# Kernel optimization log

Hardware: AMD Instinct MI355X
Metric: run time of the kernel (lower is better)

The kernel has to match this reference:

```python
import jax, jax.numpy as jnp
import numpy as np
import math

L, B, E, H = 1024, 16, 512, 8
NUM_REL = 2 * L - 1  # 2047


def setup_inputs() -> dict:
    key = jax.random.key(0)
    ks = jax.random.split(key, 9)
    s = 0.02
    query = jax.random.normal(ks[0], (L, B, E), dtype=jnp.float32)
    return {
        "query": query,
        "key": jax.random.normal(ks[1], (L, B, E), dtype=jnp.float32),
        "value": jax.random.normal(ks[2], (L, B, E), dtype=jnp.float32),
        "in_proj_weight": jax.random.normal(ks[3], (3 * E, E), dtype=jnp.float32) * s,
        "in_proj_bias": jax.random.normal(ks[4], (3 * E,), dtype=jnp.float32) * s,
        "out_proj_weight": jax.random.normal(ks[5], (E, E), dtype=jnp.float32) * s,
        "out_proj_bias": jax.random.normal(ks[6], (E,), dtype=jnp.float32) * s,
        "rpe_weight_table": jax.random.normal(ks[7], (H, NUM_REL), dtype=jnp.float32) * s,
        "rpe_indices": jax.random.randint(ks[8], (L, L), 0, NUM_REL, dtype=jnp.int32),
    }


def _heads(x, w, b):
    # x: (N, Bn, E), w: (E, E), b: (E,) -> (Bn, H, N, d)
    n, bn, e = x.shape
    d = e // H
    y = jnp.einsum('nbe,fe->nbf', x, w) + b
    return y.reshape(n, bn, H, d).transpose(1, 2, 0, 3)


def reference(query, key, value, in_proj_weight, in_proj_bias, out_proj_weight,
              out_proj_bias, rpe_weight_table, rpe_indices):
    l, bn, e = query.shape
    d = e // H
    wq, wk, wv = jnp.split(in_proj_weight, 3, axis=0)
    bq, bk, bv = jnp.split(in_proj_bias, 3, axis=0)
    q = _heads(query, wq, bq)   # (B, H, L, d)
    k = _heads(key, wk, bk)     # (B, H, S, d)
    v = _heads(value, wv, bv)   # (B, H, S, d)
    q = q / math.sqrt(d)
    # rel-pos bias: gather table -> (H, L, S), broadcast over batch
    bias = rpe_weight_table[:, rpe_indices]
    attn = jnp.einsum('bhld,bhsd->bhls', q, k) + bias[None]
    attn = jax.nn.softmax(attn, axis=-1)
    out = jnp.einsum('bhls,bhsd->bhld', attn, v)   # (B, H, L, d)
    out = out.transpose(2, 0, 1, 3).reshape(l, bn, e)  # (L, B, E)
    out = jnp.einsum('lbe,fe->lbf', out, out_proj_weight) + out_proj_bias
    return out
```

## Files before the change

### kernel.cpp

```cpp
#include <hip/hip_runtime.h>
#include <hip/hip_bf16.h>


#define L_SEQ 1024
#define B_N   16
#define E_DIM 512
#define H_N   8
#define NREL  2047

typedef _Float16 f16;
using half4   = __attribute__((ext_vector_type(4))) _Float16;
using half8   = __attribute__((ext_vector_type(8))) _Float16;
using floatx4 = __attribute__((ext_vector_type(4))) float;

#define LGKM_BARRIER() do {                                   \
    asm volatile("s_waitcnt lgkmcnt(0)" ::: "memory");        \
    __builtin_amdgcn_sched_barrier(0);                        \
    __builtin_amdgcn_s_barrier();                             \
    __builtin_amdgcn_sched_barrier(0);                        \
} while (0)

__device__ __forceinline__ half4 cvt4(const float4 a) {
    half4 h;
    h[0] = (f16)a.x; h[1] = (f16)a.y; h[2] = (f16)a.z; h[3] = (f16)a.w;
    return h;
}

__global__ __launch_bounds__(256) void qkv_kernel(
    const float* __restrict__ Xq, const float* __restrict__ Xk, const float* __restrict__ Xv,
    const float* __restrict__ W, const float* __restrict__ Bias,
    f16* __restrict__ Qo, f16* __restrict__ Ko, f16* __restrict__ Vo)
{
    const int flat = blockIdx.x;
    const int xcd  = flat & 7;
    const int slot = flat >> 3;
    const int g    = xcd * 48 + (slot >> 2);
    const int f0   = (slot & 3) << 7;
    const int proj = g >> 7;
    const int n0   = (g & 127) << 7;

    const float* X  = (proj == 0) ? Xq : (proj == 1) ? Xk : Xv;
    const float* Wp = W + (size_t)(proj << 9) * E_DIM;

    __shared__ __align__(16) f16 As[2][128][40];
    __shared__ __align__(16) f16 Bs[2][128][40];

    const int tid  = threadIdx.x;
    const int w    = tid >> 6;
    const int lane = tid & 63;
    const int quad = lane >> 4, c = lane & 15;
    const int wm = (w >> 1) << 6, wn = (w & 1) << 6;

    const int srow = (w << 5) + (lane >> 3);
    const int scol = (lane & 7) << 2;
    const float* Xg = X  + (size_t)(n0 + srow) * E_DIM + scol;
    const float* Wg = Wp + (size_t)(f0 + srow) * E_DIM + scol;

    float4 lx[4], lw[4];
    auto load_tile = [&](int kk) {
#pragma unroll
        for (int i = 0; i < 4; ++i)
            lx[i] = *reinterpret_cast<const float4*>(Xg + (size_t)(i * 8) * E_DIM + kk);
#pragma unroll
        for (int i = 0; i < 4; ++i)
            lw[i] = *reinterpret_cast<const float4*>(Wg + (size_t)(i * 8) * E_DIM + kk);
    };
    auto write_tile = [&](int buf) {
#pragma unroll
        for (int i = 0; i < 4; ++i)
            *reinterpret_cast<half4*>(&As[buf][srow + i * 8][scol]) = cvt4(lx[i]);
#pragma unroll
        for (int i = 0; i < 4; ++i)
            *reinterpret_cast<half4*>(&Bs[buf][srow + i * 8][scol]) = cvt4(lw[i]);
    };

    floatx4 acc[4][4] = {};

    load_tile(0);
    write_tile(0);
    load_tile(32);
    LGKM_BARRIER();

    for (int t = 0; t < 16; ++t) {
        const int cur = t & 1;

        half8 a[4], bfr[4];
#pragma unroll
        for (int mt = 0; mt < 4; ++mt)
            a[mt] = *reinterpret_cast<const half8*>(&As[cur][wm + mt * 16 + c][quad * 8]);
#pragma unroll
        for (int nt = 0; nt < 4; ++nt)
            bfr[nt] = *reinterpret_cast<const half8*>(&Bs[cur][wn + nt * 16 + c][quad * 8]);
#pragma unroll
        for (int mt = 0; mt < 4; ++mt)
#pragma unroll
            for (int nt = 0; nt < 4; ++nt)
                acc[mt][nt] = __builtin_amdgcn_mfma_f32_16x16x32_f16(a[mt], bfr[nt], acc[mt][nt], 0, 0, 0);

        if (t < 15) {
            write_tile(cur ^ 1);
            if (t < 14) load_tile((t + 2) * 32);
        }
        LGKM_BARRIER();
    }

    f16* Dst = (proj == 0) ? Qo : (proj == 1) ? Ko : Vo;
    const float scale = (proj == 0) ? 0.125f : 1.0f;

#pragma unroll
    for (int nt = 0; nt < 4; ++nt) {
        const int fl = f0 + wn + nt * 16 + c;
        const float bj = Bias[(proj << 9) + fl];
        const int h = fl >> 6, d = fl & 63;
#pragma unroll
        for (int mt = 0; mt < 4; ++mt) {
#pragma unroll
            for (int r = 0; r < 4; ++r) {
                const int n = n0 + wm + mt * 16 + quad * 4 + r;
                const int l = n >> 4, b = n & 15;
                Dst[((((size_t)b * H_N + h) * L_SEQ + l) << 6) + d] =
                    (f16)((acc[mt][nt][r] + bj) * scale);
            }
        }
    }
}

__global__ __launch_bounds__(256) void transpose_v(
    const f16* __restrict__ V, f16* __restrict__ Vt)
{
    const int l0 = blockIdx.x << 6;
    const size_t base = (size_t)blockIdx.y << 16;
    __shared__ __align__(16) f16 T[64][72];
    const int tid = threadIdx.x;
    const int r = tid >> 2, co = (tid & 3) << 4;

    const uint4 a0 = *reinterpret_cast<const uint4*>(V + base + (size_t)(l0 + r) * 64 + co);
    const uint4 a1 = *reinterpret_cast<const uint4*>(V + base + (size_t)(l0 + r) * 64 + co + 8);
    *reinterpret_cast<uint4*>(&T[r][co])     = a0;
    *reinterpret_cast<uint4*>(&T[r][co + 8]) = a1;
    __syncthreads();

    union { f16 h[16]; uint4 u[2]; } pk;
#pragma unroll
    for (int j = 0; j < 16; ++j) pk.h[j] = T[co + j][r];
    *reinterpret_cast<uint4*>(Vt + base + (size_t)r * 1024 + l0 + co)     = pk.u[0];
    *reinterpret_cast<uint4*>(Vt + base + (size_t)r * 1024 + l0 + co + 8) = pk.u[1];
}

__global__ __launch_bounds__(256, 3) void attn_kernel(
    const f16* __restrict__ Q, const f16* __restrict__ K, const f16* __restrict__ Vt,
    const int* __restrict__ RPE, const float* __restrict__ Tab, f16* __restrict__ CTX)
{
    const int flat = blockIdx.x;
    const int xcd  = flat & 7;
    const int slot = flat >> 3;
    const int q0   = (slot & 7) << 7;
    const int bh   = ((slot >> 3) << 3) + xcd;
    const int b = bh >> 3, h = bh & 7;

    const int tid  = threadIdx.x;
    const int w    = tid >> 6;
    const int lane = tid & 63;
    const int quad = lane >> 4, c = lane & 15;

    __shared__ __align__(16) f16 Ks[64][72];
    __shared__ __align__(16) f16 Vts[64][72];
    __shared__ __align__(16) f16 Pw[4][32][72];
    __shared__ float tab[NREL];

    const size_t base = (size_t)bh << 16;

    for (int i = tid; i < NREL; i += 256) tab[i] = Tab[h * NREL + i];

    const int qg0 = q0 + (w << 5);
    half8 Aq[2][2];
#pragma unroll
    for (int s = 0; s < 2; ++s) {
        const f16* qp = Q + base + (size_t)(qg0 + s * 16 + c) * 64 + quad * 8;
        Aq[s][0] = *reinterpret_cast<const half8*>(qp);
        Aq[s][1] = *reinterpret_cast<const half8*>(qp + 32);
    }

    floatx4 o[2][4] = {};
    float l_part[2][4] = {};

    const int* rp = RPE + (size_t)(qg0 + (quad << 2)) * 1024 + c;

    const int sr = tid >> 2, so = (tid & 3) << 4;
    const f16* kbase = K  + base + (size_t)sr * 64 + so;
    const f16* vbase = Vt + base + (size_t)sr * 1024 + so;

    uint4 pk0 = *reinterpret_cast<const uint4*>(kbase);
    uint4 pk1 = *reinterpret_cast<const uint4*>(kbase + 8);
    uint4 pv0 = *reinterpret_cast<const uint4*>(vbase);
    uint4 pv1 = *reinterpret_cast<const uint4*>(vbase + 8);

    for (int j0 = 0; j0 < L_SEQ; j0 += 64) {
        __syncthreads();
        *reinterpret_cast<uint4*>(&Ks[sr][so])      = pk0;
        *reinterpret_cast<uint4*>(&Ks[sr][so + 8])  = pk1;
        *reinterpret_cast<uint4*>(&Vts[sr][so])     = pv0;
        *reinterpret_cast<uint4*>(&Vts[sr][so + 8]) = pv1;
        __syncthreads();

        if (j0 + 64 < L_SEQ) {
            const f16* kn = kbase + (size_t)(j0 + 64) * 64;
            const f16* vn = vbase + (j0 + 64);
            pk0 = *reinterpret_cast<const uint4*>(kn);
            pk1 = *reinterpret_cast<const uint4*>(kn + 8);
            pv0 = *reinterpret_cast<const uint4*>(vn);
            pv1 = *reinterpret_cast<const uint4*>(vn + 8);
        }

        int idx[2][4][4];
#pragma unroll
        for (int s = 0; s < 2; ++s)
#pragma unroll
            for (int r = 0; r < 4; ++r)
#pragma unroll
                for (int nt = 0; nt < 4; ++nt)
                    idx[s][r][nt] = rp[(size_t)(s * 16 + r) * 1024 + j0 + nt * 16];

        floatx4 sc[2][4];
#pragma unroll
        for (int nt = 0; nt < 4; ++nt) {
            const half8 b0 = *reinterpret_cast<const half8*>(&Ks[nt * 16 + c][quad * 8]);
            const half8 b1 = *reinterpret_cast<const half8*>(&Ks[nt * 16 + c][32 + quad * 8]);
            floatx4 t0 = {}, t1 = {};
            t0 = __builtin_amdgcn_mfma_f32_16x16x32_f16(Aq[0][0], b0, t0, 0, 0, 0);
            t0 = __builtin_amdgcn_mfma_f32_16x16x32_f16(Aq[0][1], b1, t0, 0, 0, 0);
            t1 = __builtin_amdgcn_mfma_f32_16x16x32_f16(Aq[1][0], b0, t1, 0, 0, 0);
            t1 = __builtin_amdgcn_mfma_f32_16x16x32_f16(Aq[1][1], b1, t1, 0, 0, 0);
            sc[0][nt] = t0; sc[1][nt] = t1;
        }

#pragma unroll
        for (int s = 0; s < 2; ++s)
#pragma unroll
            for (int r = 0; r < 4; ++r) {
                float rs = 0.0f;
#pragma unroll
                for (int nt = 0; nt < 4; ++nt) {
                    const float p = __expf(sc[s][nt][r] + tab[idx[s][r][nt]]);
                    rs += p;
                    Pw[w][s * 16 + quad * 4 + r][nt * 16 + c] = (f16)p;
                }
                l_part[s][r] += rs;
            }

        half8 vb[4][2];
#pragma unroll
        for (int nt = 0; nt < 4; ++nt) {
            vb[nt][0] = *reinterpret_cast<const half8*>(&Vts[nt * 16 + c][quad * 8]);
            vb[nt][1] = *reinterpret_cast<const half8*>(&Vts[nt * 16 + c][32 + quad * 8]);
        }
#pragma unroll
        for (int s = 0; s < 2; ++s) {
            const half8 Ap0 = *reinterpret_cast<const half8*>(&Pw[w][s * 16 + c][quad * 8]);
            const half8 Ap1 = *reinterpret_cast<const half8*>(&Pw[w][s * 16 + c][32 + quad * 8]);
#pragma unroll
            for (int nt = 0; nt < 4; ++nt) {
                o[s][nt] = __builtin_amdgcn_mfma_f32_16x16x32_f16(Ap0, vb[nt][0], o[s][nt], 0, 0, 0);
                o[s][nt] = __builtin_amdgcn_mfma_f32_16x16x32_f16(Ap1, vb[nt][1], o[s][nt], 0, 0, 0);
            }
        }
    }

#pragma unroll
    for (int s = 0; s < 2; ++s)
#pragma unroll
        for (int r = 0; r < 4; ++r) {
            float l = l_part[s][r];
            l += __shfl_xor(l, 1); l += __shfl_xor(l, 2);
            l += __shfl_xor(l, 4); l += __shfl_xor(l, 8);
            const float inv = 1.0f / l;
            const int lrow = qg0 + s * 16 + quad * 4 + r;
            f16* dp = CTX + ((size_t)(lrow * 16 + b)) * 512 + h * 64;
#pragma unroll
            for (int nt = 0; nt < 4; ++nt)
                dp[nt * 16 + c] = (f16)(o[s][nt][r] * inv);
        }
}

__global__ __launch_bounds__(256) void out_kernel(
    const f16* __restrict__ X, const float* __restrict__ W, const float* __restrict__ Bias,
    float* __restrict__ Out)
{
    const int flat = blockIdx.x;
    const int xcd  = flat & 7;
    const int slot = flat >> 3;
    const int m    = xcd * 16 + (slot >> 2);
    const int f0   = (slot & 3) << 7;
    const int n0   = m << 7;

    __shared__ __align__(16) f16 As[2][128][40];
    __shared__ __align__(16) f16 Bs[2][128][40];

    const int tid  = threadIdx.x;
    const int w    = tid >> 6;
    const int lane = tid & 63;
    const int quad = lane >> 4, c = lane & 15;
    const int wm = (w >> 1) << 6, wn = (w & 1) << 6;

    const int arow = (w << 5) + (lane >> 2);
    const int acol = (lane & 3) << 3;
    const f16* Xg = X + (size_t)(n0 + arow) * E_DIM + acol;

    const int srow = (w << 5) + (lane >> 3);
    const int scol = (lane & 7) << 2;
    const float* Wg = W + (size_t)(f0 + srow) * E_DIM + scol;

    uint4  la[2];
    float4 lw[4];
    auto load_tile = [&](int kk) {
#pragma unroll
        for (int i = 0; i < 2; ++i)
            la[i] = *reinterpret_cast<const uint4*>(Xg + (size_t)(i * 16) * E_DIM + kk);
#pragma unroll
        for (int i = 0; i < 4; ++i)
            lw[i] = *reinterpret_cast<const float4*>(Wg + (size_t)(i * 8) * E_DIM + kk);
    };
    auto write_tile = [&](int buf) {
#pragma unroll
        for (int i = 0; i < 2; ++i)
            *reinterpret_cast<uint4*>(&As[buf][arow + i * 16][acol]) = la[i];
#pragma unroll
        for (int i = 0; i < 4; ++i)
            *reinterpret_cast<half4*>(&Bs[buf][srow + i * 8][scol]) = cvt4(lw[i]);
    };

    floatx4 acc[4][4] = {};

    load_tile(0);
    write_tile(0);
    load_tile(32);
    LGKM_BARRIER();

    for (int t = 0; t < 16; ++t) {
        const int cur = t & 1;

        half8 a[4], bfr[4];
#pragma unroll
        for (int mt = 0; mt < 4; ++mt)
            a[mt] = *reinterpret_cast<const half8*>(&As[cur][wm + mt * 16 + c][quad * 8]);
#pragma unroll
        for (int nt = 0; nt < 4; ++nt)
            bfr[nt] = *reinterpret_cast<const half8*>(&Bs[cur][wn + nt * 16 + c][quad * 8]);
#pragma unroll
        for (int mt = 0; mt < 4; ++mt)
#pragma unroll
            for (int nt = 0; nt < 4; ++nt)
                acc[mt][nt] = __builtin_amdgcn_mfma_f32_16x16x32_f16(a[mt], bfr[nt], acc[mt][nt], 0, 0, 0);

        if (t < 15) {
            write_tile(cur ^ 1);
            if (t < 14) load_tile((t + 2) * 32);
        }
        LGKM_BARRIER();
    }

#pragma unroll
    for (int nt = 0; nt < 4; ++nt) {
        const int f = f0 + wn + nt * 16 + c;
        const float bj = Bias[f];
#pragma unroll
        for (int mt = 0; mt < 4; ++mt) {
#pragma unroll
            for (int r = 0; r < 4; ++r) {
                const int n = n0 + wm + mt * 16 + quad * 4 + r;
                Out[(size_t)n * E_DIM + f] = acc[mt][nt][r] + bj;
            }
        }
    }
}

extern "C" void kernel_launch(void* const* d_in, const int* in_sizes, int n_in,
                              void* d_out, int out_size, void* d_ws, size_t ws_size,
                              hipStream_t stream) {
    const float* q_in = (const float*)d_in[0];
    const float* k_in = (const float*)d_in[1];
    const float* v_in = (const float*)d_in[2];
    const float* ipw  = (const float*)d_in[3];
    const float* ipb  = (const float*)d_in[4];
    const float* opw  = (const float*)d_in[5];
    const float* opb  = (const float*)d_in[6];
    const float* tab  = (const float*)d_in[7];
    const int*   rpe  = (const int*)d_in[8];
    float* out = (float*)d_out;

    f16* ws   = (f16*)d_ws;
    f16* Q    = ws;
    f16* K    = ws + 8388608;
    f16* Vt   = ws + 16777216;
    f16* Vtmp = ws + 25165824;
    f16* CTX  = ws + 25165824;

    qkv_kernel<<<dim3(1536), 256, 0, stream>>>(q_in, k_in, v_in, ipw, ipb, Q, K, Vtmp);
    transpose_v<<<dim3(16, 128), 256, 0, stream>>>(Vtmp, Vt);
    attn_kernel<<<dim3(1024), 256, 0, stream>>>(Q, K, Vt, rpe, tab, CTX);
    out_kernel<<<dim3(512), 256, 0, stream>>>(CTX, opw, opb, out);
}
```

Measured before the change: 308.9 us.

## Precompute RPE bias in fragment-ordered fp16 layout, drop in-loop table gather

Adds a pre-pass kernel that gathers the relative-position table by the index matrix for all heads. It stores the bias as fp16 in a layout that matches each lane's MFMA accumulator fragment. The attention kernel then prefetches this bias with wide vector loads alongside K/V, replacing the per-iteration int index loads and LDS table lookups, and drops the LDS table. This frees LDS and registers, so launch bounds are raised to 4 waves-groups per CU. The cost is an extra launch, a 16 MB bias buffer write and read, and fp16 rounding of the bias.

```diff
diff --git a/kernel.cpp b/kernel.cpp
--- a/kernel.cpp
+++ b/kernel.cpp
@@ -24,6 +24,49 @@
     half4 h;
     h[0] = (f16)a.x; h[1] = (f16)a.y; h[2] = (f16)a.z; h[3] = (f16)a.w;
     return h;
+}
+
+__global__ __launch_bounds__(256) void rpe_expand(
+    const int* __restrict__ RPE, const float* __restrict__ Tab, f16* __restrict__ EB)
+{
+    const int qg = blockIdx.x;
+    const int jt = blockIdx.y;
+    __shared__ float tabs[H_N * NREL];
+    const int tid = threadIdx.x;
+    for (int i = tid; i < H_N * NREL; i += 256) tabs[i] = Tab[i];
+
+    const int w = tid >> 6, lane = tid & 63;
+    const int quad = lane >> 4, c = lane & 15;
+
+    const int* rp = RPE + (size_t)(qg * 32 + quad * 4) * 1024 + jt * 64 + c;
+    int id[2][4][4];
+#pragma unroll
+    for (int s = 0; s < 2; ++s)
+#pragma unroll
+        for (int r = 0; r < 4; ++r)
+#pragma unroll
+            for (int nt = 0; nt < 4; ++nt)
+                id[s][r][nt] = rp[(size_t)(s * 16 + r) * 1024 + nt * 16];
+
+    __syncthreads();
+
+#pragma unroll
+    for (int hh = 0; hh < 2; ++hh) {
+        const int h = w * 2 + hh;
+        union { f16 v[32]; uint4 u[4]; } o;
+#pragma unroll
+        for (int s = 0; s < 2; ++s)
+#pragma unroll
+            for (int nt = 0; nt < 4; ++nt)
+#pragma unroll
+                for (int r = 0; r < 4; ++r)
+                    o.v[s * 16 + nt * 4 + r] = (f16)tabs[h * NREL + id[s][r][nt]];
+
+        f16* dst = EB + ((((size_t)h * 32 + qg) * 16 + jt) << 11) + lane * 32;
+#pragma unroll
+        for (int i = 0; i < 4; ++i)
+            *reinterpret_cast<uint4*>(dst + i * 8) = o.u[i];
+    }
 }
 
 __global__ __launch_bounds__(256) void qkv_kernel(
@@ -147,9 +190,9 @@
     *reinterpret_cast<uint4*>(Vt + base + (size_t)r * 1024 + l0 + co + 8) = pk.u[1];
 }
 
-__global__ __launch_bounds__(256, 3) void attn_kernel(
+__global__ __launch_bounds__(256, 4) void attn_kernel(
     const f16* __restrict__ Q, const f16* __restrict__ K, const f16* __restrict__ Vt,
-    const int* __restrict__ RPE, const float* __restrict__ Tab, f16* __restrict__ CTX)
+    const f16* __restrict__ EB, f16* __restrict__ CTX)
 {
     const int flat = blockIdx.x;
     const int xcd  = flat & 7;
@@ -166,11 +209,8 @@
     __shared__ __align__(16) f16 Ks[64][72];
     __shared__ __align__(16) f16 Vts[64][72];
     __shared__ __align__(16) f16 Pw[4][32][72];
-    __shared__ float tab[NREL];
 
     const size_t base = (size_t)bh << 16;
-
-    for (int i = tid; i < NREL; i += 256) tab[i] = Tab[h * NREL + i];
 
     const int qg0 = q0 + (w << 5);
     half8 Aq[2][2];
@@ -184,7 +224,7 @@
     floatx4 o[2][4] = {};
     float l_part[2][4] = {};
 
-    const int* rp = RPE + (size_t)(qg0 + (quad << 2)) * 1024 + c;
+    const f16* ebp = EB + ((((size_t)h * 32 + (q0 >> 5) + w) * 16) << 11) + (size_t)lane * 32;
 
     const int sr = tid >> 2, so = (tid & 3) << 4;
     const f16* kbase = K  + base + (size_t)sr * 64 + so;
@@ -194,6 +234,10 @@
     uint4 pk1 = *reinterpret_cast<const uint4*>(kbase + 8);
     uint4 pv0 = *reinterpret_cast<const uint4*>(vbase);
     uint4 pv1 = *reinterpret_cast<const uint4*>(vbase + 8);
+    uint4 pe[4];
+#pragma unroll
+    for (int i = 0; i < 4; ++i)
+        pe[i] = *reinterpret_cast<const uint4*>(ebp + i * 8);
 
     for (int j0 = 0; j0 < L_SEQ; j0 += 64) {
         __syncthreads();
@@ -203,6 +247,10 @@
         *reinterpret_cast<uint4*>(&Vts[sr][so + 8]) = pv1;
         __syncthreads();
 
+        union { uint4 u[4]; half8 h[4]; } eb;
+#pragma unroll
+        for (int i = 0; i < 4; ++i) eb.u[i] = pe[i];
+
         if (j0 + 64 < L_SEQ) {
             const f16* kn = kbase + (size_t)(j0 + 64) * 64;
             const f16* vn = vbase + (j0 + 64);
@@ -210,16 +258,11 @@
             pk1 = *reinterpret_cast<const uint4*>(kn + 8);
             pv0 = *reinterpret_cast<const uint4*>(vn);
             pv1 = *reinterpret_cast<const uint4*>(vn + 8);
-        }
-
-        int idx[2][4][4];
-#pragma unroll
-        for (int s = 0; s < 2; ++s)
-#pragma unroll
-            for (int r = 0; r < 4; ++r)
-#pragma unroll
-                for (int nt = 0; nt < 4; ++nt)
-                    idx[s][r][nt] = rp[(size_t)(s * 16 + r) * 1024 + j0 + nt * 16];
+            const f16* en = ebp + (size_t)(j0 / 64 + 1) * 2048;
+#pragma unroll
+            for (int i = 0; i < 4; ++i)
+                pe[i] = *reinterpret_cast<const uint4*>(en + i * 8);
+        }
 
         floatx4 sc[2][4];
 #pragma unroll
@@ -241,7 +284,8 @@
                 float rs = 0.0f;
 #pragma unroll
                 for (int nt = 0; nt < 4; ++nt) {
-                    const float p = __expf(sc[s][nt][r] + tab[idx[s][r][nt]]);
+                    const float bias = (float)eb.h[s * 2 + (nt >> 1)][(nt & 1) * 4 + r];
+                    const float p = __expf(sc[s][nt][r] + bias);
                     rs += p;
                     Pw[w][s * 16 + quad * 4 + r][nt * 16 + c] = (f16)p;
                 }
@@ -394,9 +438,11 @@
     f16* Vt   = ws + 16777216;
     f16* Vtmp = ws + 25165824;
     f16* CTX  = ws + 25165824;
-
+    f16* EB   = ws + 33554432;
+
+    rpe_expand<<<dim3(32, 16), 256, 0, stream>>>(rpe, tab, EB);
     qkv_kernel<<<dim3(1536), 256, 0, stream>>>(q_in, k_in, v_in, ipw, ipb, Q, K, Vtmp);
     transpose_v<<<dim3(16, 128), 256, 0, stream>>>(Vtmp, Vt);
-    attn_kernel<<<dim3(1024), 256, 0, stream>>>(Q, K, Vt, rpe, tab, CTX);
+    attn_kernel<<<dim3(1024), 256, 0, stream>>>(Q, K, Vt, EB, CTX);
     out_kernel<<<dim3(512), 256, 0, stream>>>(CTX, opw, opb, out);
 }
```

Measured after the change: 388.5 us. 1.26x slower.
